# Performance work log

Hardware: AMD Instinct MI355X
Metric: run time of the kernel (lower is better)

The kernel has to match this reference:

```python
import jax, jax.numpy as jnp
import numpy as np

NUM_ITERATIONS = 3


def squash(v, axis=-1):
    sq = jnp.sum(v * v, axis=axis, keepdims=True)
    scale = sq / (1.0 + sq)
    return scale * v / jnp.sqrt(sq)


def setup_inputs() -> dict:
    key = jax.random.key(0)
    k1, k2 = jax.random.split(key)
    B, N, IN, OUT, CAPS = 512, 4608, 16, 32, 32
    x = jax.random.normal(k1, (B, N, IN), dtype=jnp.float32)
    # torch.rand -> uniform [0, 1)
    route_weights = jax.random.uniform(k2, (N, IN, OUT), dtype=jnp.float32)
    return {"x": x, "route_weights": route_weights, "num_capsules": CAPS}


def reference(x, route_weights, num_capsules):
    # x: [B, N, IN], route_weights: [N, IN, OUT]
    u_hat = jnp.einsum('bnk,nkl->bnl', x, route_weights)  # [B, N, OUT]
    N = x.shape[1]
    b = jnp.zeros((N, num_capsules), dtype=u_hat.dtype)  # routing logits [N, CAPS]
    v = None
    for it in range(NUM_ITERATIONS):
        c = jax.nn.softmax(b, axis=-1)                     # [N, CAPS]
        s = jnp.einsum('bnk,nc->bck', u_hat, c)            # [B, CAPS, OUT]
        v = squash(s, axis=-1)                             # [B, CAPS, OUT]
        if it < NUM_ITERATIONS - 1:
            b = b + jnp.einsum('bnk,bck->nc', u_hat, v)    # agreement, reduced over batch
    return v
```

## Files before the change

kernel.cpp:

```cpp
#include <hip/hip_runtime.h>


#define NB 512
#define KTOT 73728
#define OUTC 32
#define NCAPS 32

#define KSPLIT 128
#define KCHUNK (KTOT / KSPLIT)
#define NTILE 9
#define SPA_BYTES ((size_t)KSPLIT * NB * OUTC * 4)
#define S_BYTES ((size_t)NB * OUTC * 4)

typedef short bf16x8 __attribute__((ext_vector_type(8)));
typedef float f32x4 __attribute__((ext_vector_type(4)));

__device__ __forceinline__ unsigned int f2bf(float f) {
    union { float f; unsigned int u; } v; v.f = f;
    unsigned int u = v.u;
    return (u + 0x7fffu + ((u >> 16) & 1u)) >> 16;
}

template <bool PART>
__global__ __launch_bounds__(256) void gemm_mfma(
        const float* __restrict__ x, const float* __restrict__ w,
        float* __restrict__ S) {
    __shared__ __align__(16) unsigned short wl[2048];
    __shared__ __align__(16) unsigned short xl[4096];
    const int t = threadIdx.x;
    const int lane = t & 63;
    const int wave = t >> 6;
    const int bx = blockIdx.x;
    const int by = blockIdx.y;
    const int brow = by * 64;
    const size_t kbase = (size_t)bx * KCHUNK;

    const int m = lane & 15;
    const int q = lane >> 4;

    const int sm_ = t & 15;
    const int sr_ = t >> 4;
    const int xsl = sm_ >> 3;
    const int xq  = (sm_ >> 1) & 3;
    const int xj0 = (sm_ & 1) * 4;
    const int ll  = t & 63;
    const int h   = (t >> 6) & 1;
    const int slw = t >> 7;
    const int wk0 = slw * 32 + ((ll >> 4) & 3) * 8;
    const int wc  = h * 16 + (ll & 15);

    f32x4 acc0 = {0.f, 0.f, 0.f, 0.f};
    f32x4 acc1 = {0.f, 0.f, 0.f, 0.f};

    float  wr[8];
    float4 xr[4];

    {
        const float* wp0 = w + (kbase + (size_t)wk0) * OUTC + wc;
#pragma unroll
        for (int j = 0; j < 8; ++j) wr[j] = wp0[(size_t)j * OUTC];
        const float* xb = x + kbase + sm_ * 4;
#pragma unroll
        for (int ld = 0; ld < 4; ++ld)
            xr[ld] = *(const float4*)(xb + (size_t)(brow + sr_ + ld * 16) * KTOT);
    }

    for (int tile = 0; tile < NTILE; ++tile) {
        {
            unsigned int u0 = f2bf(wr[0]) | (f2bf(wr[1]) << 16);
            unsigned int u1 = f2bf(wr[2]) | (f2bf(wr[3]) << 16);
            unsigned int u2 = f2bf(wr[4]) | (f2bf(wr[5]) << 16);
            unsigned int u3 = f2bf(wr[6]) | (f2bf(wr[7]) << 16);
            *(uint4*)&wl[t * 8] = make_uint4(u0, u1, u2, u3);
#pragma unroll
            for (int ld = 0; ld < 4; ++ld) {
                unsigned int a0 = f2bf(xr[ld].x) | (f2bf(xr[ld].y) << 16);
                unsigned int a1 = f2bf(xr[ld].z) | (f2bf(xr[ld].w) << 16);
                *(uint2*)&xl[((ld * 2 + xsl) * 16 + sr_) * 32 + xq * 8 + xj0] =
                    make_uint2(a0, a1);
            }
        }
        if (tile + 1 < NTILE) {
            const size_t kt = kbase + (size_t)(tile + 1) * 64;
            const float* wp0 = w + (kt + (size_t)wk0) * OUTC + wc;
#pragma unroll
            for (int j = 0; j < 8; ++j) wr[j] = wp0[(size_t)j * OUTC];
            const float* xb = x + kt + sm_ * 4;
#pragma unroll
            for (int ld = 0; ld < 4; ++ld)
                xr[ld] = *(const float4*)(xb + (size_t)(brow + sr_ + ld * 16) * KTOT);
        }
        __syncthreads();
#pragma unroll
        for (int sl = 0; sl < 2; ++sl) {
            bf16x8 a  = *(const bf16x8*)&xl[((wave * 2 + sl) * 16 + m) * 32 + q * 8];
            bf16x8 b0 = *(const bf16x8*)&wl[sl * 1024 + lane * 8];
            bf16x8 b1 = *(const bf16x8*)&wl[sl * 1024 + 512 + lane * 8];
            acc0 = __builtin_amdgcn_mfma_f32_16x16x32_bf16(a, b0, acc0, 0, 0, 0);
            acc1 = __builtin_amdgcn_mfma_f32_16x16x32_bf16(a, b1, acc1, 0, 0, 0);
        }
        __syncthreads();
    }

    const int row0 = brow + wave * 16;
#pragma unroll
    for (int r = 0; r < 4; ++r) {
        const int row = row0 + q * 4 + r;
        if (PART) {
            float* dst = S + ((size_t)bx * NB + row) * OUTC;
            dst[m] = acc0[r];
            dst[16 + m] = acc1[r];
        } else {
            atomicAdd(&S[(size_t)row * OUTC + m], acc0[r]);
            atomicAdd(&S[(size_t)row * OUTC + 16 + m], acc1[r]);
        }
    }
}

__global__ __launch_bounds__(256) void zero_s(float* __restrict__ S) {
    int i = blockIdx.x * 256 + threadIdx.x;
    if (i < NB * OUTC) S[i] = 0.0f;
}

__global__ __launch_bounds__(256) void finalize2(const float* __restrict__ S,
                                                 float* __restrict__ out) {
    __shared__ float sm[8][32];
    const int b = blockIdx.x;
    const int t = threadIdx.x;
    const int k = t & 31;
    const int g = t >> 5;
    const float* sp = S + ((size_t)(g * 16) * NB + b) * OUTC + k;
    float a = 0.0f;
#pragma unroll 16
    for (int i = 0; i < 16; ++i)
        a += sp[(size_t)i * NB * OUTC];
    sm[g][k] = a;
    __syncthreads();
    float tot = 0.0f;
#pragma unroll
    for (int gg = 0; gg < 8; ++gg) tot += sm[gg][k];
    float s = tot * (1.0f / 32.0f);
    float sq = s * s;
    sq += __shfl_xor(sq, 16, 64);
    sq += __shfl_xor(sq, 8, 64);
    sq += __shfl_xor(sq, 4, 64);
    sq += __shfl_xor(sq, 2, 64);
    sq += __shfl_xor(sq, 1, 64);
    float scale = sq / ((1.0f + sq) * sqrtf(sq));
    float v = s * scale;
    float* orow = out + (size_t)b * (NCAPS * OUTC);
#pragma unroll
    for (int j = 0; j < 4; ++j)
        orow[(g * 4 + j) * OUTC + k] = v;
}

__global__ __launch_bounds__(64) void finalize_k(const float* __restrict__ S,
                                                 float* __restrict__ out) {
    const int b = blockIdx.x;
    const int t = threadIdx.x;
    const int k = t & 31;
    const int h = t >> 5;
    float s = S[(size_t)b * OUTC + k] * (1.0f / 32.0f);
    float sq = s * s;
    sq += __shfl_xor(sq, 16, 64);
    sq += __shfl_xor(sq, 8, 64);
    sq += __shfl_xor(sq, 4, 64);
    sq += __shfl_xor(sq, 2, 64);
    sq += __shfl_xor(sq, 1, 64);
    float scale = sq / ((1.0f + sq) * sqrtf(sq));
    float v = s * scale;
    float* orow = out + (size_t)b * (NCAPS * OUTC);
#pragma unroll
    for (int j = 0; j < 16; ++j)
        orow[(h + j * 2) * OUTC + k] = v;
}

#define FKSPLIT 64
#define FKCHUNK 1152
#define FKT 128
#define FNQ 32
#define FRPW 2
#define FKSTR 132

__global__ __launch_bounds__(256) void gemm_fb(
        const float* __restrict__ x, const float* __restrict__ w,
        float* __restrict__ S) {
    __shared__ float wlds[OUTC * FKSTR];
    const int t = threadIdx.x;
    const int lane = t & 63;
    const int l32 = lane & 31;
    const int half = lane >> 5;
    const int wave = t >> 6;
    const int row0 = blockIdx.x * 16 + wave * 4 + half * FRPW;
    const size_t kbase = (size_t)blockIdx.y * FKCHUNK;
    const int sc = t & 31;
    const int sh = t >> 5;

    float acc[FRPW][OUTC];
#pragma unroll
    for (int r = 0; r < FRPW; ++r)
#pragma unroll
        for (int c = 0; c < OUTC; ++c) acc[r][c] = 0.0f;

    const float4* xq[FRPW];
#pragma unroll
    for (int r = 0; r < FRPW; ++r)
        xq[r] = (const float4*)(x + (size_t)(row0 + r) * KTOT + kbase);

    for (int tile = 0; tile < FKCHUNK / FKT; ++tile) {
        float4 xv[FRPW];
#pragma unroll
        for (int r = 0; r < FRPW; ++r)
            xv[r] = xq[r][tile * FNQ + l32];
#pragma unroll
        for (int jj = 0; jj < 4; ++jj) {
            int kk = 4 * (jj * 8 + sh);
            const float* wg = w + (kbase + (size_t)tile * FKT + kk) * OUTC + sc;
            *(float4*)&wlds[sc * FKSTR + kk] =
                make_float4(wg[0], wg[OUTC], wg[2 * OUTC], wg[3 * OUTC]);
        }
        __syncthreads();
#pragma unroll
        for (int c = 0; c < OUTC; ++c) {
            float4 wv = *(const float4*)&wlds[c * FKSTR + 4 * l32];
#pragma unroll
            for (int r = 0; r < FRPW; ++r) {
                float a = acc[r][c];
                a = fmaf(xv[r].x, wv.x, a);
                a = fmaf(xv[r].y, wv.y, a);
                a = fmaf(xv[r].z, wv.z, a);
                a = fmaf(xv[r].w, wv.w, a);
                acc[r][c] = a;
            }
        }
        __syncthreads();
    }
#pragma unroll
    for (int r = 0; r < FRPW; ++r) {
        float myv = 0.0f;
#pragma unroll
        for (int c = 0; c < OUTC; ++c) {
            float v = acc[r][c];
            v += __shfl_xor(v, 16, 64);
            v += __shfl_xor(v, 8, 64);
            v += __shfl_xor(v, 4, 64);
            v += __shfl_xor(v, 2, 64);
            v += __shfl_xor(v, 1, 64);
            if (l32 == c) myv = v;
        }
        atomicAdd(&S[(size_t)(row0 + r) * OUTC + l32], myv);
    }
}

extern "C" void kernel_launch(void* const* d_in, const int* in_sizes, int n_in,
                              void* d_out, int out_size, void* d_ws, size_t ws_size,
                              hipStream_t stream) {
    const float* x = (const float*)d_in[0];
    const float* w = (const float*)d_in[1];
    float* out = (float*)d_out;

    if (ws_size >= SPA_BYTES) {
        float* S = (float*)d_ws;
        hipLaunchKernelGGL((gemm_mfma<true>), dim3(KSPLIT, 8), dim3(256), 0,
                           stream, x, w, S);
        hipLaunchKernelGGL(finalize2, dim3(NB), dim3(256), 0, stream, S, out);
    } else if (ws_size >= S_BYTES) {
        float* S = (float*)d_ws;
        hipLaunchKernelGGL(zero_s, dim3((NB * OUTC + 255) / 256), dim3(256), 0,
                           stream, S);
        hipLaunchKernelGGL((gemm_mfma<false>), dim3(KSPLIT, 8), dim3(256), 0,
                           stream, x, w, S);
        hipLaunchKernelGGL(finalize_k, dim3(NB), dim3(64), 0, stream, S, out);
    } else {
        float* S = (float*)d_ws;
        hipLaunchKernelGGL(zero_s, dim3((NB * OUTC + 255) / 256), dim3(256), 0,
                           stream, S);
        hipLaunchKernelGGL(gemm_fb, dim3(32, FKSPLIT), dim3(256), 0, stream,
                           x, w, S);
        hipLaunchKernelGGL(finalize_k, dim3(NB), dim3(64), 0, stream, S, out);
    }
}
```

Before: 224.3 us.

## Double-buffer LDS tiles in MFMA GEMM and drop one barrier per tile

```diff
diff --git a/kernel.cpp b/kernel.cpp
--- a/kernel.cpp
+++ b/kernel.cpp
@@ -22,11 +22,11 @@
 }
 
 template <bool PART>
-__global__ __launch_bounds__(256) void gemm_mfma(
+__global__ __launch_bounds__(256, 6) void gemm_mfma(
         const float* __restrict__ x, const float* __restrict__ w,
         float* __restrict__ S) {
-    __shared__ __align__(16) unsigned short wl[2048];
-    __shared__ __align__(16) unsigned short xl[4096];
+    __shared__ __align__(16) unsigned short wl[2][2048];
+    __shared__ __align__(16) unsigned short xl[2][4096];
     const int t = threadIdx.x;
     const int lane = t & 63;
     const int wave = t >> 6;
@@ -49,58 +49,63 @@
     const int wk0 = slw * 32 + ((ll >> 4) & 3) * 8;
     const int wc  = h * 16 + (ll & 15);
 
+    float  wr[8];
+    float4 xr[4];
+
+#define LOADT(T) do {                                                        \
+        const size_t kt = kbase + (size_t)(T) * 64;                          \
+        const float* wp0 = w + (kt + (size_t)wk0) * OUTC + wc;               \
+        _Pragma("unroll")                                                    \
+        for (int j = 0; j < 8; ++j) wr[j] = wp0[(size_t)j * OUTC];           \
+        const float* xb = x + kt + sm_ * 4;                                  \
+        _Pragma("unroll")                                                    \
+        for (int ld = 0; ld < 4; ++ld)                                       \
+            xr[ld] = *(const float4*)(xb +                                   \
+                        (size_t)(brow + sr_ + ld * 16) * KTOT);              \
+    } while (0)
+
+#define WRITET(T) do {                                                       \
+        const int bw_ = (T) & 1;                                             \
+        unsigned int u0 = f2bf(wr[0]) | (f2bf(wr[1]) << 16);                 \
+        unsigned int u1 = f2bf(wr[2]) | (f2bf(wr[3]) << 16);                 \
+        unsigned int u2 = f2bf(wr[4]) | (f2bf(wr[5]) << 16);                 \
+        unsigned int u3 = f2bf(wr[6]) | (f2bf(wr[7]) << 16);                 \
+        *(uint4*)&wl[bw_][t * 8] = make_uint4(u0, u1, u2, u3);               \
+        _Pragma("unroll")                                                    \
+        for (int ld = 0; ld < 4; ++ld) {                                     \
+            unsigned int a0 = f2bf(xr[ld].x) | (f2bf(xr[ld].y) << 16);       \
+            unsigned int a1 = f2bf(xr[ld].z) | (f2bf(xr[ld].w) << 16);       \
+            *(uint2*)&xl[bw_][((ld * 2 + xsl) * 16 + sr_) * 32               \
+                              + xq * 8 + xj0] = make_uint2(a0, a1);          \
+        }                                                                    \
+    } while (0)
+
     f32x4 acc0 = {0.f, 0.f, 0.f, 0.f};
     f32x4 acc1 = {0.f, 0.f, 0.f, 0.f};
 
-    float  wr[8];
-    float4 xr[4];
-
-    {
-        const float* wp0 = w + (kbase + (size_t)wk0) * OUTC + wc;
-#pragma unroll
-        for (int j = 0; j < 8; ++j) wr[j] = wp0[(size_t)j * OUTC];
-        const float* xb = x + kbase + sm_ * 4;
-#pragma unroll
-        for (int ld = 0; ld < 4; ++ld)
-            xr[ld] = *(const float4*)(xb + (size_t)(brow + sr_ + ld * 16) * KTOT);
-    }
+    LOADT(0);
+    WRITET(0);
+    LOADT(1);
+    __syncthreads();
 
     for (int tile = 0; tile < NTILE; ++tile) {
-        {
-            unsigned int u0 = f2bf(wr[0]) | (f2bf(wr[1]) << 16);
-            unsigned int u1 = f2bf(wr[2]) | (f2bf(wr[3]) << 16);
-            unsigned int u2 = f2bf(wr[4]) | (f2bf(wr[5]) << 16);
-            unsigned int u3 = f2bf(wr[6]) | (f2bf(wr[7]) << 16);
-            *(uint4*)&wl[t * 8] = make_uint4(u0, u1, u2, u3);
-#pragma unroll
-            for (int ld = 0; ld < 4; ++ld) {
-                unsigned int a0 = f2bf(xr[ld].x) | (f2bf(xr[ld].y) << 16);
-                unsigned int a1 = f2bf(xr[ld].z) | (f2bf(xr[ld].w) << 16);
-                *(uint2*)&xl[((ld * 2 + xsl) * 16 + sr_) * 32 + xq * 8 + xj0] =
-                    make_uint2(a0, a1);
-            }
-        }
-        if (tile + 1 < NTILE) {
-            const size_t kt = kbase + (size_t)(tile + 1) * 64;
-            const float* wp0 = w + (kt + (size_t)wk0) * OUTC + wc;
-#pragma unroll
-            for (int j = 0; j < 8; ++j) wr[j] = wp0[(size_t)j * OUTC];
-            const float* xb = x + kt + sm_ * 4;
-#pragma unroll
-            for (int ld = 0; ld < 4; ++ld)
-                xr[ld] = *(const float4*)(xb + (size_t)(brow + sr_ + ld * 16) * KTOT);
-        }
-        __syncthreads();
+        const int buf = tile & 1;
 #pragma unroll
         for (int sl = 0; sl < 2; ++sl) {
-            bf16x8 a  = *(const bf16x8*)&xl[((wave * 2 + sl) * 16 + m) * 32 + q * 8];
-            bf16x8 b0 = *(const bf16x8*)&wl[sl * 1024 + lane * 8];
-            bf16x8 b1 = *(const bf16x8*)&wl[sl * 1024 + 512 + lane * 8];
+            bf16x8 a  = *(const bf16x8*)&xl[buf][((wave * 2 + sl) * 16 + m) * 32 + q * 8];
+            bf16x8 b0 = *(const bf16x8*)&wl[buf][sl * 1024 + lane * 8];
+            bf16x8 b1 = *(const bf16x8*)&wl[buf][sl * 1024 + 512 + lane * 8];
             acc0 = __builtin_amdgcn_mfma_f32_16x16x32_bf16(a, b0, acc0, 0, 0, 0);
             acc1 = __builtin_amdgcn_mfma_f32_16x16x32_bf16(a, b1, acc1, 0, 0, 0);
         }
-        __syncthreads();
-    }
+        if (tile + 1 < NTILE) {
+            WRITET(tile + 1);
+            if (tile + 2 < NTILE) LOADT(tile + 2);
+            __syncthreads();
+        }
+    }
+#undef LOADT
+#undef WRITET
 
     const int row0 = brow + wave * 16;
 #pragma unroll
```

New measurement: 224.8 us. No clear change (+0.2%).
